# Kernel tuning notes

Measured on AMD Instinct MI355X. Metric: run time of the kernel, lower is better.

Reference implementation:

```python
import jax, jax.numpy as jnp
import numpy as np
import math
from jax import lax

CANVAS = 300.0
NUM_CLASSES = 80
SCORE_THR = 0.01
K_CAND = 400   # candidates kept per image before NMS (cfg cltop=400)
K_OUT = 200    # final detections per image
IOU_THR = 0.45
CLIP = math.log(1000.0 / 16.0)  # exp clamp in decode_boxes
_FSIZES = [38, 19, 10, 5, 3, 1]
_STRIDES = [8, 16, 32, 64, 100, 300]
_SCALES = [0.07, 0.15, 0.33, 0.51, 0.69, 0.87, 1.05]
_AR3 = [1, 2, 3]
_ANUMS = [4, 6, 6, 6, 4, 4]


def _make_priors():
    # SSD300 priors (tv config: no rounding, clamp to canvas), cxcywh, [8732,4]
    out = []
    for i, (st, fs) in enumerate(zip(_STRIDES, _FSIZES)):
        s = _SCALES[i] * 300.0
        e = math.sqrt(_SCALES[i] * _SCALES[i + 1]) * 300.0
        ratios = [2.0, 0.5] + ([3.0, 1.0 / 3.0] if i in _AR3 else [])
        wh = [(s, s), (e, e)] + [(s * math.sqrt(r), s / math.sqrt(r)) for r in ratios]
        wh = np.array([(min(w, 300.0), min(h, 300.0)) for w, h in wh], np.float32)
        cy, cx = np.meshgrid(np.arange(fs), np.arange(fs), indexing='ij')
        ctr = np.stack([(cx + 0.5) * st, (cy + 0.5) * st], -1).reshape(-1, 2).astype(np.float32)
        A = wh.shape[0]
        out.append(np.concatenate([np.repeat(ctr, A, 0), np.tile(wh, (fs * fs, 1))], 1))
    return np.concatenate(out, 0)


def _head(x, w, b, tl):
    # Conv2d(c, an*tl, 3, 1, 1) -> permute(0,2,3,1) -> reshape(B, -1, tl)
    y = lax.conv_general_dilated(x, w, (1, 1), [(1, 1), (1, 1)],
                                 dimension_numbers=('NCHW', 'OIHW', 'NCHW'))
    y = y + b[None, :, None, None]
    n = y.shape[0]
    return jnp.transpose(y, (0, 2, 3, 1)).reshape(n, -1, tl)


def _decode(deltas, pri):
    cx = pri[:, 0] + deltas[:, 0] * 0.1 * pri[:, 2]
    cy = pri[:, 1] + deltas[:, 1] * 0.1 * pri[:, 3]
    w = pri[:, 2] * jnp.exp(jnp.minimum(deltas[:, 2] * 0.2, CLIP))
    h = pri[:, 3] * jnp.exp(jnp.minimum(deltas[:, 3] * 0.2, CLIP))
    b = jnp.stack([cx - 0.5 * w, cy - 0.5 * h, cx + 0.5 * w, cy + 0.5 * h], -1)
    return jnp.clip(b, 0.0, CANVAS)  # clamp_to_canvas


def _pairwise_iou(b):
    area = (b[:, 2] - b[:, 0]) * (b[:, 3] - b[:, 1])
    lt = jnp.maximum(b[:, None, :2], b[None, :, :2])
    rb = jnp.minimum(b[:, None, 2:], b[None, :, 2:])
    wh = jnp.clip(rb - lt, 0.0)
    inter = wh[..., 0] * wh[..., 1]
    return inter / (area[:, None] + area[None, :] - inter + 1e-9)


def _post_one(scr, reg, priors):
    # scr [A, C] (background already dropped), reg [A, 4]
    C = scr.shape[1]
    flat = jnp.where(scr > SCORE_THR, scr, 0.0).reshape(-1)
    s, idx = lax.top_k(flat, K_CAND)          # sorted desc -> greedy NMS order
    cls = idx % C + 1                          # bckg_class_first=False -> +1
    anc = idx // C
    boxes = _decode(reg[anc], priors[anc])
    valid = (s > 0.0) & (boxes[:, 2] > boxes[:, 0]) & (boxes[:, 3] > boxes[:, 1])
    s = jnp.where(valid, s, 0.0)
    # class-aware NMS via per-class coordinate offset (batched_nms trick)
    off = cls.astype(boxes.dtype)[:, None] * (CANVAS + 1.0)
    iou = _pairwise_iou(boxes + off)
    def body(i, keep):
        sup = (iou[i] > IOU_THR) & (jnp.arange(K_CAND) > i) & keep[i]
        return keep & (~sup)
    keep = lax.fori_loop(0, K_CAND, body, valid)
    fs, fi = lax.top_k(jnp.where(keep, s, 0.0), K_OUT)
    return boxes[fi], fs, jnp.where(fs > 0.0, cls[fi], 0).astype(jnp.int32)


def setup_inputs() -> dict:
    key = jax.random.key(0)
    shapes = [(16, 512, 38, 38), (16, 1024, 19, 19), (16, 512, 10, 10),
              (16, 256, 5, 5), (16, 256, 3, 3), (16, 256, 1, 1)]
    d = {}
    k = key
    for i, (shp, an) in enumerate(zip(shapes, _ANUMS)):
        c = shp[1]
        k, k1, k2, k3 = jax.random.split(k, 4)
        d['feat%d' % i] = jax.random.normal(k1, shp, jnp.float32)
        d['cls_w%d' % i] = jax.random.normal(k2, (an * (NUM_CLASSES + 1), c, 3, 3), jnp.float32) * 0.03
        d['cls_b%d' % i] = jnp.zeros((an * (NUM_CLASSES + 1),), jnp.float32)
        d['reg_w%d' % i] = jax.random.normal(k3, (an * 4, c, 3, 3), jnp.float32) * 0.03
        d['reg_b%d' % i] = jnp.zeros((an * 4,), jnp.float32)
    d['priors'] = jnp.asarray(_make_priors())
    return d


def reference(feat0, feat1, feat2, feat3, feat4, feat5,
              cls_w0, cls_b0, cls_w1, cls_b1, cls_w2, cls_b2,
              cls_w3, cls_b3, cls_w4, cls_b4, cls_w5, cls_b5,
              reg_w0, reg_b0, reg_w1, reg_b1, reg_w2, reg_b2,
              reg_w3, reg_b3, reg_w4, reg_b4, reg_w5, reg_b5,
              priors):
    feats = [feat0, feat1, feat2, feat3, feat4, feat5]
    cws = [cls_w0, cls_w1, cls_w2, cls_w3, cls_w4, cls_w5]
    cbs = [cls_b0, cls_b1, cls_b2, cls_b3, cls_b4, cls_b5]
    rws = [reg_w0, reg_w1, reg_w2, reg_w3, reg_w4, reg_w5]
    rbs = [reg_b0, reg_b1, reg_b2, reg_b3, reg_b4, reg_b5]
    cls = jnp.concatenate([_head(f, w, b, NUM_CLASSES + 1) for f, w, b in zip(feats, cws, cbs)], 1)
    reg = jnp.concatenate([_head(f, w, b, 4) for f, w, b in zip(feats, rws, rbs)], 1)
    scr = jax.nn.softmax(cls, axis=-1)[:, :, 1:]  # drop background (class 0)
    boxes, scores, classes = jax.vmap(_post_one, in_axes=(0, 0, None))(scr, reg, priors)
    return boxes, scores, classes
```

## Files before the change

### kernel.cpp

```cpp
#include <hip/hip_runtime.h>
#include <math.h>
#include <stdint.h>

#define NIMG 16
#define A_TOTAL 8732
#define NCLS 80
#define TL_CLS 81
#define CANVASF 300.0f
#define SCORE_THR 0.01f
#define IOU_THRF 0.45f
#define KCAND 400
#define KOUT 200
#define CAND_CAP 4096
#define NBIN 65536

typedef double d4 __attribute__((ext_vector_type(4)));

__device__ __forceinline__ float clampf(float v, float lo, float hi) {
    return fminf(fmaxf(v, lo), hi);
}

struct ConvJobs {
    const float* feat[6];
    const float* wgtT[6];
    const float* biasC[6];
    const float* biasR[6];
    float* outc;
    float* outr;
    int Cin[6], lgC[6], Hd[6], Mtot[6], Mcls[6], Mp[6], an[6], off[6];
    int mW[6], jobTiles[6];
    int cum[8][7];
    int cs[8][6];
};

struct TransJobs {
    const float* srcC[6];
    const float* srcR[6];
    float* dst[6];
    int Cin[6], K[6], Mcls[6], Mtot[6], Mp[6], mT[6], start[6];
    int total;
};

__global__ __launch_bounds__(256) void transpose_wgt(TransJobs tj)
{
    __shared__ float lds[32][33];
    int bid = (int)blockIdx.x;
    int L = 0;
    while (L + 1 < 6 && bid >= tj.start[L + 1]) L++;
    int rel = bid - tj.start[L];
    int mTi = rel % tj.mT[L];
    int kTi = rel / tj.mT[L];
    int m0 = mTi * 32, k0 = kTi * 32;
    const int K = tj.K[L];
    const int tid = threadIdx.x;

    {
        int ml = tid >> 3;
        int kq = (tid & 7) << 2;
        int m = m0 + ml;
        float4 v = make_float4(0.f, 0.f, 0.f, 0.f);
        if (m < tj.Mcls[L])
            v = *(const float4*)(tj.srcC[L] + (size_t)m * K + k0 + kq);
        else if (m < tj.Mtot[L])
            v = *(const float4*)(tj.srcR[L] + (size_t)(m - tj.Mcls[L]) * K + k0 + kq);
        lds[kq + 0][ml] = v.x;
        lds[kq + 1][ml] = v.y;
        lds[kq + 2][ml] = v.z;
        lds[kq + 3][ml] = v.w;
    }
    __syncthreads();
    {
        int kk = tid >> 3;
        int mq = (tid & 7) << 2;
        int k = k0 + kk;
        int ci = k / 9;
        int r = k - ci * 9;
        int kp = r * tj.Cin[L] + ci;
        float4 w;
        w.x = lds[kk][mq + 0];
        w.y = lds[kk][mq + 1];
        w.z = lds[kk][mq + 2];
        w.w = lds[kk][mq + 3];
        *(float4*)(tj.dst[L] + (size_t)kp * tj.Mp[L] + m0 + mq) = w;
    }
}

__device__ __forceinline__ void conv_wave(
    const float* __restrict__ feat, const float* __restrict__ wgtT,
    const float* __restrict__ biasC, const float* __restrict__ biasR,
    float* __restrict__ outc, float* __restrict__ outr,
    int Cin, int lgC, int Hd, int Mtot, int Mcls, int Mp, int an, int lvl_off,
    int n0, int m0)
{
    const int K = Cin * 9;
    const int HW = Hd * Hd;
    const int N = NIMG * HW;
    const int CHW = Cin * HW;
    const int lane = threadIdx.x & 63;
    const int lm = lane & 15;
    const int lk = lane >> 4;

    int rowIdx[4], colIdx[4];
    {
        d4 z = (d4){0.0, 0.0, 0.0, 0.0};
        d4 pr = __builtin_amdgcn_mfma_f64_16x16x4f64((double)lm, 1.0, z, 0, 0, 0);
        d4 pc = __builtin_amdgcn_mfma_f64_16x16x4f64(1.0, (double)lm, z, 0, 0, 0);
#pragma unroll
        for (int i = 0; i < 4; i++) {
            rowIdx[i] = (int)(pr[i] * 0.25 + 0.5);
            colIdx[i] = (int)(pc[i] * 0.25 + 0.5);
        }
    }

    const int gPerR = Cin >> 2;
    const int KBg = K >> 2;

    int voffA = lk * Mp + m0 + lm;
    int voffB[4];
    float maskc[4];
    float bufA[4][2], bufB[4][4], bufM[4][4];

    d4 acc[2][4];
#pragma unroll
    for (int a = 0; a < 2; a++)
#pragma unroll
        for (int c = 0; c < 4; c++) acc[a][c] = (d4){0.0, 0.0, 0.0, 0.0};

    auto newR = [&](int r) {
        int ky = (r * 171) >> 9;
        int kx = r - 3 * ky;
#pragma unroll
        for (int c = 0; c < 4; c++) {
            int ng = n0 + lm + 16 * c;
            bool nv = ng < N;
            int bimg = 0, p = 0;
            if (nv) { bimg = ng / HW; p = ng - bimg * HW; }
            int y0 = p / Hd;
            int x0 = p - y0 * Hd;
            int yy = y0 + ky - 1;
            int xx = x0 + kx - 1;
            bool v = nv && (yy >= 0) && (yy < Hd) && (xx >= 0) && (xx < Hd);
            maskc[c] = v ? 1.0f : 0.0f;
            voffB[c] = bimg * CHW + lk * HW + (v ? (yy * Hd + xx) : 0);
        }
    };

    auto loadG = [&](int g, int slot) {
        if ((g & (gPerR - 1)) == 0) newR(g >> (lgC - 2));
#pragma unroll
        for (int c = 0; c < 4; c++) {
            bufB[slot][c] = feat[voffB[c]];
            bufM[slot][c] = maskc[c];
            voffB[c] += 4 * HW;
        }
        bufA[slot][0] = wgtT[voffA];
        bufA[slot][1] = wgtT[voffA + 16];
        voffA += 4 * Mp;
    };

    loadG(0, 0);
    loadG(1, 1);
    loadG(2, 2);
    loadG(3, 3);
    for (int g = 0; g < KBg; g += 4) {
#pragma unroll
        for (int u = 0; u < 4; u++) {
            double a0 = (double)bufA[u][0];
            double a1 = (double)bufA[u][1];
            double b0 = (double)(bufB[u][0] * bufM[u][0]);
            double b1 = (double)(bufB[u][1] * bufM[u][1]);
            double b2 = (double)(bufB[u][2] * bufM[u][2]);
            double b3 = (double)(bufB[u][3] * bufM[u][3]);
            if (g + 4 + u < KBg) loadG(g + 4 + u, u);
            acc[0][0] = __builtin_amdgcn_mfma_f64_16x16x4f64(a0, b0, acc[0][0], 0, 0, 0);
            acc[1][0] = __builtin_amdgcn_mfma_f64_16x16x4f64(a1, b0, acc[1][0], 0, 0, 0);
            acc[0][1] = __builtin_amdgcn_mfma_f64_16x16x4f64(a0, b1, acc[0][1], 0, 0, 0);
            acc[1][1] = __builtin_amdgcn_mfma_f64_16x16x4f64(a1, b1, acc[1][1], 0, 0, 0);
            acc[0][2] = __builtin_amdgcn_mfma_f64_16x16x4f64(a0, b2, acc[0][2], 0, 0, 0);
            acc[1][2] = __builtin_amdgcn_mfma_f64_16x16x4f64(a1, b2, acc[1][2], 0, 0, 0);
            acc[0][3] = __builtin_amdgcn_mfma_f64_16x16x4f64(a0, b3, acc[0][3], 0, 0, 0);
            acc[1][3] = __builtin_amdgcn_mfma_f64_16x16x4f64(a1, b3, acc[1][3], 0, 0, 0);
        }
    }

#pragma unroll
    for (int mi2 = 0; mi2 < 2; mi2++)
#pragma unroll
    for (int c = 0; c < 4; c++)
#pragma unroll
    for (int i = 0; i < 4; i++) {
        int mg = m0 + mi2 * 16 + rowIdx[i];
        int ng2 = n0 + c * 16 + colIdx[i];
        if (mg >= Mtot || ng2 >= N) continue;
        int b = ng2 / HW;
        int p = ng2 - b * HW;
        double val = acc[mi2][c][i];
        if (mg < Mcls) {
            int aidx = mg / TL_CLS;
            int t = mg - aidx * TL_CLS;
            int row = lvl_off + p * an + aidx;
            outc[((size_t)b * A_TOTAL + row) * TL_CLS + t] = (float)(val + (double)biasC[mg]);
        } else {
            int rm = mg - Mcls;
            int aidx = rm >> 2;
            int t = rm & 3;
            int row = lvl_off + p * an + aidx;
            outr[((size_t)b * A_TOTAL + row) * 4 + t] = (float)(val + (double)biasR[rm]);
        }
    }
}

__global__ __launch_bounds__(256, 4) void fused_conv(ConvJobs J)
{
    int bid = (int)blockIdx.x;
    int x = bid & 7;
    int r = bid >> 3;
    if (r >= J.cum[x][6]) return;
    int j = 0;
    while (j + 1 < 6 && r >= J.cum[x][j + 1]) j++;
    int blkInJob = J.cs[x][j] + (r - J.cum[x][j]);

    int wave = threadIdx.x >> 6;
    int tile = blkInJob * 4 + wave;
    if (tile >= J.jobTiles[j]) return;
    int mt = tile % J.mW[j];
    int nt = tile / J.mW[j];

    conv_wave(J.feat[j], J.wgtT[j], J.biasC[j], J.biasR[j], J.outc, J.outr,
              J.Cin[j], J.lgC[j], J.Hd[j], J.Mtot[j], J.Mcls[j], J.Mp[j],
              J.an[j], J.off[j], nt * 64, mt * 32);
}

__global__ __launch_bounds__(256) void softmax_kernel(
    const float* __restrict__ cls, float* __restrict__ scr,
    unsigned int* __restrict__ hist, int nrows)
{
    __shared__ float buf[64 * 81];
    __shared__ float inv[64];
    const int row0 = blockIdx.x * 64;
    const int tid = threadIdx.x;

    for (int i = tid; i < 64 * 81; i += 256) {
        int r = row0 + i / 81;
        buf[i] = (r < nrows) ? cls[(size_t)row0 * 81 + i] : 0.0f;
    }
    __syncthreads();
    if (tid < 64) {
        float m = -1e30f;
        for (int c = 0; c < 81; c++) m = fmaxf(m, buf[tid * 81 + c]);
        double md = (double)m;
        double ssum = 0.0;
        for (int c = 0; c < 81; c++) {
            double e = exp((double)buf[tid * 81 + c] - md);
            buf[tid * 81 + c] = (float)e;
            ssum += e;
        }
        inv[tid] = (float)(1.0 / ssum);
    }
    __syncthreads();
    for (int i = tid; i < 64 * 80; i += 256) {
        int r = i / 80;
        int c = i - r * 80;
        int gr = row0 + r;
        if (gr < nrows) {
            float v = buf[r * 81 + c + 1] * inv[r];
            scr[(size_t)gr * 80 + c] = v;
            if (v > SCORE_THR) {
                int img = gr / A_TOTAL;
                atomicAdd(&hist[img * NBIN + (__float_as_uint(v) >> 16)], 1u);
            }
        }
    }
}

__global__ void zero_kernel(unsigned int* __restrict__ p, int n)
{
    int i = blockIdx.x * blockDim.x + threadIdx.x;
    if (i < n) p[i] = 0u;
}

__global__ __launch_bounds__(1024) void select_kernel(
    const unsigned int* __restrict__ hist, unsigned int* __restrict__ sel)
{
    __shared__ unsigned int ps[1024];
    __shared__ int s_found;
    const int img = blockIdx.x;
    const int tid = threadIdx.x;

    unsigned int p = 0;
    const int base = img * NBIN + tid * 64;
    for (int j = 0; j < 64; j++) p += hist[base + j];
    ps[tid] = p;
    if (tid == 0) s_found = 0;
    __syncthreads();

    for (int off = 1; off < 1024; off <<= 1) {
        unsigned int v = (tid + off < 1024) ? ps[tid + off] : 0u;
        __syncthreads();
        ps[tid] += v;
        __syncthreads();
    }

    unsigned int St = ps[tid];
    unsigned int Sn = (tid < 1023) ? ps[tid + 1] : 0u;
    if (St >= KCAND && (tid == 1023 || Sn < KCAND)) {
        unsigned int cum = Sn;
        int b0 = 0;
        for (int b = tid * 64 + 63; b >= tid * 64; b--) {
            cum += hist[img * NBIN + b];
            if (cum >= KCAND) { b0 = b; break; }
        }
        sel[img] = (unsigned int)b0;
        s_found = 1;
    }
    __syncthreads();
    if (tid == 0 && !s_found) sel[img] = 0u;
}

__global__ void gather_kernel(const float* __restrict__ scr,
                              const unsigned int* __restrict__ sel,
                              unsigned int* __restrict__ candcnt,
                              uint2* __restrict__ cand)
{
    const int per_img = A_TOTAL * NCLS;
    const size_t total = (size_t)NIMG * per_img;
    for (size_t i = (size_t)blockIdx.x * blockDim.x + threadIdx.x; i < total;
         i += (size_t)gridDim.x * blockDim.x) {
        float v = scr[i];
        if (v > SCORE_THR) {
            int img = (int)(i / per_img);
            unsigned int u = __float_as_uint(v);
            if ((u >> 16) >= sel[img]) {
                unsigned int pos = atomicAdd(&candcnt[img], 1u);
                if (pos < CAND_CAP) {
                    unsigned int ridx = (unsigned int)(i - (size_t)img * per_img);
                    cand[(size_t)img * CAND_CAP + pos] = make_uint2(u, ridx);
                }
            }
        }
    }
}

__global__ __launch_bounds__(1024) void nms_kernel(
    const uint2* __restrict__ cand, const unsigned int* __restrict__ candcnt,
    const float* __restrict__ reg_all, const float* __restrict__ priors,
    float* __restrict__ out)
{
    __shared__ unsigned long long key[CAND_CAP];
    __shared__ float s_sc[KCAND];
    __shared__ float s_bx[KCAND][4];
    __shared__ float s_ob[KCAND][4];
    __shared__ float s_ar[KCAND];
    __shared__ float s_cl[KCAND];
    __shared__ int s_keep[KCAND];
    __shared__ int s_fi[KOUT];

    const int img = blockIdx.x;
    const int tid = threadIdx.x;
    unsigned int craw = candcnt[img];
    const int cnt = (craw > CAND_CAP) ? CAND_CAP : (int)craw;

    for (int i = tid; i < CAND_CAP; i += 1024) {
        unsigned long long kv = 0ull;
        if (i < cnt) {
            uint2 e = cand[(size_t)img * CAND_CAP + i];
            kv = ((unsigned long long)e.x << 32) | (unsigned int)(~e.y);
        }
        key[i] = kv;
    }
    __syncthreads();

    for (int ksz = 2; ksz <= CAND_CAP; ksz <<= 1) {
        for (int jj = ksz >> 1; jj > 0; jj >>= 1) {
            for (int i = tid; i < CAND_CAP; i += 1024) {
                int p = i ^ jj;
                if (p > i) {
                    bool desc = ((i & ksz) == 0);
                    unsigned long long a = key[i];
                    unsigned long long b = key[p];
                    bool sw = desc ? (a < b) : (a > b);
                    if (sw) { key[i] = b; key[p] = a; }
                }
            }
            __syncthreads();
        }
    }

    const float CLIPF = 4.135166556742356f;
    if (tid < KCAND) {
        const int j = tid;
        float s = 0.0f;
        unsigned int idx = 0u;
        if (j < cnt) {
            unsigned long long kv = key[j];
            unsigned int bits = (unsigned int)(kv >> 32);
            idx = ~((unsigned int)kv);
            s = __uint_as_float(bits);
        }
        int anc = (int)(idx / NCLS);
        int cl = (int)(idx - (unsigned int)anc * NCLS) + 1;
        const float* d = reg_all + ((size_t)img * A_TOTAL + anc) * 4;
        const float* pr = priors + (size_t)anc * 4;
        float d0 = d[0], d1 = d[1], d2 = d[2], d3 = d[3];
        float p0 = pr[0], p1 = pr[1], p2 = pr[2], p3 = pr[3];
        float cx = p0 + d0 * 0.1f * p2;
        float cy = p1 + d1 * 0.1f * p3;
        float t2 = fminf(d2 * 0.2f, CLIPF);
        float t3 = fminf(d3 * 0.2f, CLIPF);
        float bw = p2 * (float)exp((double)t2);
        float bh = p3 * (float)exp((double)t3);
        float x1 = clampf(cx - 0.5f * bw, 0.0f, CANVASF);
        float y1 = clampf(cy - 0.5f * bh, 0.0f, CANVASF);
        float x2 = clampf(cx + 0.5f * bw, 0.0f, CANVASF);
        float y2 = clampf(cy + 0.5f * bh, 0.0f, CANVASF);
        bool valid = (s > 0.0f) && (x2 > x1) && (y2 > y1);
        s = valid ? s : 0.0f;
        float off = (float)cl * (CANVASF + 1.0f);
        float ox1 = x1 + off, oy1 = y1 + off, ox2 = x2 + off, oy2 = y2 + off;
        s_sc[j] = s;
        s_cl[j] = (float)cl;
        s_keep[j] = valid ? 1 : 0;
        s_bx[j][0] = x1; s_bx[j][1] = y1; s_bx[j][2] = x2; s_bx[j][3] = y2;
        s_ob[j][0] = ox1; s_ob[j][1] = oy1; s_ob[j][2] = ox2; s_ob[j][3] = oy2;
        s_ar[j] = (ox2 - ox1) * (oy2 - oy1);
    }
    __syncthreads();

    for (int i = 0; i < KCAND; i++) {
        int ki = s_keep[i];
        if (ki && tid < KCAND && tid > i) {
            float lx = fmaxf(s_ob[i][0], s_ob[tid][0]);
            float ly = fmaxf(s_ob[i][1], s_ob[tid][1]);
            float rx = fminf(s_ob[i][2], s_ob[tid][2]);
            float ry = fminf(s_ob[i][3], s_ob[tid][3]);
            float iw = fmaxf(rx - lx, 0.0f);
            float ih = fmaxf(ry - ly, 0.0f);
            float inter = iw * ih;
            float iou = inter / (s_ar[i] + s_ar[tid] - inter + 1e-9f);
            if (iou > IOU_THRF) s_keep[tid] = 0;
        }
        __syncthreads();
    }

    if (tid == 0) {
        int pos = 0;
        for (int j = 0; j < KCAND && pos < KOUT; j++)
            if (s_keep[j]) s_fi[pos++] = j;
        for (int j = 0; j < KCAND && pos < KOUT; j++)
            if (!s_keep[j]) s_fi[pos++] = j;
    }
    __syncthreads();

    if (tid < KOUT) {
        int j = s_fi[tid];
        float fs = s_keep[j] ? s_sc[j] : 0.0f;
        size_t o = (size_t)img * KOUT + tid;
        out[o * 4 + 0] = s_bx[j][0];
        out[o * 4 + 1] = s_bx[j][1];
        out[o * 4 + 2] = s_bx[j][2];
        out[o * 4 + 3] = s_bx[j][3];
        out[(size_t)NIMG * KOUT * 4 + o] = fs;
        out[(size_t)NIMG * KOUT * 5 + o] = (fs > 0.0f) ? s_cl[j] : 0.0f;
    }
}

extern "C" void kernel_launch(void* const* d_in, const int* in_sizes, int n_in,
                              void* d_out, int out_size, void* d_ws, size_t ws_size,
                              hipStream_t stream)
{
    static const int Cin_[6] = {512, 1024, 512, 256, 256, 256};
    static const int lgC_[6] = {9, 10, 9, 8, 8, 8};
    static const int HW_[6]  = {38, 19, 10, 5, 3, 1};
    static const int an_[6]  = {4, 6, 6, 6, 4, 4};
    static const int off_[6] = {0, 5776, 7942, 8542, 8692, 8728};
    static const int Mp_[6]  = {352, 512, 512, 512, 352, 352};
    static const size_t wOffF_[6] = {0, 1622016, 6340608, 8699904, 0, 9879552};

    char* ws = (char*)d_ws;
    const size_t OFF_CLS  = 0;
    const size_t OFF_SCR  = 45266688;
    const size_t OFF_REG  = 89974528;
    const size_t OFF_HIST = 92209920;
    const size_t OFF_CCNT = 96404224;
    const size_t OFF_SEL  = 96404288;
    const size_t OFF_CAND = 96404352;

    float* cls_all = (float*)(ws + OFF_CLS);
    float* scr     = (float*)(ws + OFF_SCR);
    float* reg_all = (float*)(ws + OFF_REG);
    unsigned int* hist    = (unsigned int*)(ws + OFF_HIST);
    unsigned int* candcnt = (unsigned int*)(ws + OFF_CCNT);
    unsigned int* sel     = (unsigned int*)(ws + OFF_SEL);
    uint2* cand           = (uint2*)(ws + OFF_CAND);

    float* wT = scr;
    float* hT = (float*)hist;

    {
        TransJobs tj;
        int ts = 0;
        for (int L = 0; L < 6; L++) {
            tj.srcC[L] = (const float*)d_in[L * 5 + 1];
            tj.srcR[L] = (const float*)d_in[L * 5 + 3];
            tj.dst[L] = (L == 4) ? hT : (wT + wOffF_[L]);
            tj.Cin[L] = Cin_[L];
            tj.K[L] = Cin_[L] * 9;
            tj.Mcls[L] = an_[L] * TL_CLS;
            tj.Mtot[L] = an_[L] * 85;
            tj.Mp[L] = Mp_[L];
            tj.mT[L] = Mp_[L] / 32;
            tj.start[L] = ts;
            ts += (Mp_[L] / 32) * (Cin_[L] * 9 / 32);
        }
        tj.total = ts;
        transpose_wgt<<<ts, 256, 0, stream>>>(tj);
    }

    ConvJobs jobs;
    static const int ord_lvl[6] = {1, 0, 2, 3, 4, 5};
    int Bj[6];
    for (int q = 0; q < 6; q++) {
        int L = ord_lvl[q];
        int an = an_[L];
        jobs.feat[q]  = (const float*)d_in[L * 5 + 0];
        jobs.wgtT[q]  = (L == 4) ? hT : (wT + wOffF_[L]);
        jobs.biasC[q] = (const float*)d_in[L * 5 + 2];
        jobs.biasR[q] = (const float*)d_in[L * 5 + 4];
        jobs.Cin[q]   = Cin_[L];
        jobs.lgC[q]   = lgC_[L];
        jobs.Hd[q]    = HW_[L];
        jobs.Mcls[q]  = an * TL_CLS;
        jobs.Mtot[q]  = an * 85;
        jobs.Mp[q]    = Mp_[L];
        jobs.an[q]    = an;
        jobs.off[q]   = off_[L];
        int N = NIMG * HW_[L] * HW_[L];
        int nT = (N + 63) / 64;
        int mW = (jobs.Mtot[q] + 31) / 32;
        jobs.mW[q] = mW;
        jobs.jobTiles[q] = nT * mW;
        Bj[q] = (nT * mW + 3) / 4;
    }
    int maxT = 0;
    for (int x = 0; x < 8; x++) {
        int acc = 0;
        for (int q = 0; q < 6; q++) {
            int s = (int)(((long long)x * Bj[q]) / 8);
            int e = (int)(((long long)(x + 1) * Bj[q]) / 8);
            jobs.cs[x][q] = s;
            jobs.cum[x][q] = acc;
            acc += e - s;
        }
        jobs.cum[x][6] = acc;
        if (acc > maxT) maxT = acc;
    }
    jobs.outc = cls_all;
    jobs.outr = reg_all;

    fused_conv<<<8 * maxT, 256, 0, stream>>>(jobs);

    {
        int nz = NIMG * NBIN + 16 + 16;
        zero_kernel<<<(nz + 255) / 256, 256, 0, stream>>>(hist, nz);
    }

    softmax_kernel<<<(NIMG * A_TOTAL + 63) / 64, 256, 0, stream>>>(
        cls_all, scr, hist, NIMG * A_TOTAL);
    select_kernel<<<NIMG, 1024, 0, stream>>>(hist, sel);
    gather_kernel<<<2048, 256, 0, stream>>>(scr, sel, candcnt, cand);
    nms_kernel<<<NIMG, 1024, 0, stream>>>(cand, candcnt, reg_all,
                                          (const float*)d_in[30], (float*)d_out);
}
```

Baseline: 4.142 ms.

## Shrink conv prefetch depth to three and parallelize softmax max/exp across threads

The conv wave's software prefetch ring drops from four to three stages and the launch-bounds occupancy hint goes from 4 to 3 blocks per CU, trading latency hiding for register headroom. The softmax kernel now spreads the row max and the double-precision exp over all 256 threads (4 per row) using a double shared buffer, where before only 64 threads did serial per-row loops. The sum stays serial per row. The double shared buffer raises LDS use per block, and the exp values are now kept in double before being cast to float.

```diff
diff --git a/kernel.cpp b/kernel.cpp
--- a/kernel.cpp
+++ b/kernel.cpp
@@ -118,7 +118,7 @@
     int voffA = lk * Mp + m0 + lm;
     int voffB[4];
     float maskc[4];
-    float bufA[4][2], bufB[4][4], bufM[4][4];
+    float bufA[3][2], bufB[3][4], bufM[3][4];
 
     d4 acc[2][4];
 #pragma unroll
@@ -161,17 +161,16 @@
     loadG(0, 0);
     loadG(1, 1);
     loadG(2, 2);
-    loadG(3, 3);
-    for (int g = 0; g < KBg; g += 4) {
-#pragma unroll
-        for (int u = 0; u < 4; u++) {
+    for (int g = 0; g < KBg; g += 3) {
+#pragma unroll
+        for (int u = 0; u < 3; u++) {
             double a0 = (double)bufA[u][0];
             double a1 = (double)bufA[u][1];
             double b0 = (double)(bufB[u][0] * bufM[u][0]);
             double b1 = (double)(bufB[u][1] * bufM[u][1]);
             double b2 = (double)(bufB[u][2] * bufM[u][2]);
             double b3 = (double)(bufB[u][3] * bufM[u][3]);
-            if (g + 4 + u < KBg) loadG(g + 4 + u, u);
+            if (g + 3 + u < KBg) loadG(g + 3 + u, u);
             acc[0][0] = __builtin_amdgcn_mfma_f64_16x16x4f64(a0, b0, acc[0][0], 0, 0, 0);
             acc[1][0] = __builtin_amdgcn_mfma_f64_16x16x4f64(a1, b0, acc[1][0], 0, 0, 0);
             acc[0][1] = __builtin_amdgcn_mfma_f64_16x16x4f64(a0, b1, acc[0][1], 0, 0, 0);
@@ -210,7 +209,7 @@
     }
 }
 
-__global__ __launch_bounds__(256, 4) void fused_conv(ConvJobs J)
+__global__ __launch_bounds__(256, 3) void fused_conv(ConvJobs J)
 {
     int bid = (int)blockIdx.x;
     int x = bid & 7;
@@ -235,26 +234,35 @@
     const float* __restrict__ cls, float* __restrict__ scr,
     unsigned int* __restrict__ hist, int nrows)
 {
-    __shared__ float buf[64 * 81];
+    __shared__ double ebuf[64][81];
+    __shared__ double pmax[64][4];
     __shared__ float inv[64];
     const int row0 = blockIdx.x * 64;
     const int tid = threadIdx.x;
 
     for (int i = tid; i < 64 * 81; i += 256) {
-        int r = row0 + i / 81;
-        buf[i] = (r < nrows) ? cls[(size_t)row0 * 81 + i] : 0.0f;
+        int r = i / 81;
+        int c = i - r * 81;
+        int gr = row0 + r;
+        ebuf[r][c] = (gr < nrows) ? (double)cls[(size_t)row0 * 81 + i] : 0.0;
+    }
+    __syncthreads();
+    {
+        int r = tid >> 2, q = tid & 3;
+        double m = -1e30;
+        for (int c = q; c < 81; c += 4) m = fmax(m, ebuf[r][c]);
+        pmax[r][q] = m;
+    }
+    __syncthreads();
+    {
+        int r = tid >> 2, q = tid & 3;
+        double md = fmax(fmax(pmax[r][0], pmax[r][1]), fmax(pmax[r][2], pmax[r][3]));
+        for (int c = q; c < 81; c += 4) ebuf[r][c] = exp(ebuf[r][c] - md);
     }
     __syncthreads();
     if (tid < 64) {
-        float m = -1e30f;
-        for (int c = 0; c < 81; c++) m = fmaxf(m, buf[tid * 81 + c]);
-        double md = (double)m;
         double ssum = 0.0;
-        for (int c = 0; c < 81; c++) {
-            double e = exp((double)buf[tid * 81 + c] - md);
-            buf[tid * 81 + c] = (float)e;
-            ssum += e;
-        }
+        for (int c = 0; c < 81; c++) ssum += ebuf[tid][c];
         inv[tid] = (float)(1.0 / ssum);
     }
     __syncthreads();
@@ -263,7 +271,7 @@
         int c = i - r * 80;
         int gr = row0 + r;
         if (gr < nrows) {
-            float v = buf[r * 81 + c + 1] * inv[r];
+            float v = (float)ebuf[r][c + 1] * inv[r];
             scr[(size_t)gr * 80 + c] = v;
             if (v > SCORE_THR) {
                 int img = gr / A_TOTAL;
```

Measured after the change: 3.698 ms. -10.7%, faster.
